# Kernel optimization log

Measured on AMD Instinct MI355X. Metric: run time of the kernel, lower is better.

The kernel has to match this reference:

```python
import jax, jax.numpy as jnp
import numpy as np

K = 16  # top-k affinities kept per current-frame pixel (init arg k)


def setup_inputs() -> dict:
    key = jax.random.key(0)
    k1, k2 = jax.random.split(key)
    B, C, H, W = 2, 256, 64, 64
    N = H * W
    cur_prev_aff = jax.random.normal(k1, (B, N, N), dtype=jnp.float32)
    feat = jax.random.normal(k2, (B, C, H, W), dtype=jnp.float32)
    return {"cur_prev_aff": cur_prev_aff, "feat": feat}


def reference(cur_prev_aff, feat):
    # cur_prev_aff: [B, N, N] affinity from each current pixel i to each prev pixel j
    # feat:         [B, C, H, W] previous-frame features, N = H*W
    B, C, H, W = feat.shape
    N = H * W
    # top-k affinity masking per current pixel
    vals, idx = jax.lax.top_k(cur_prev_aff, K)      # [B, N, K]
    w = jax.nn.softmax(vals, axis=-1)               # normalized masked affinities (masked_cpa)
    # gather prev-frame features at top-k locations and weighted-sum
    feat_t = feat.reshape(B, C, N).transpose(0, 2, 1)        # [B, N, C]
    gathered = jax.vmap(lambda f, ix: f[ix])(feat_t, idx)    # [B, N, K, C]
    out = jnp.einsum('bnk,bnkc->bnc', w, gathered)           # [B, N, C]
    return out.transpose(0, 2, 1).reshape(B, C, H, W)
```

## Files before the change

### kernel.cpp

```cpp
#include <hip/hip_runtime.h>

#define N_PIX 4096
#define N_CH 256
#define KSEL 16
#define SCAP 64

__device__ __forceinline__ unsigned f2key(float f) {
  unsigned u = __float_as_uint(f);
  return u ^ ((unsigned)((int)u >> 31) | 0x80000000u);
}
__device__ __forceinline__ float key2f(unsigned k) {
  unsigned u = (k & 0x80000000u) ? (k ^ 0x80000000u) : ~k;
  return __uint_as_float(u);
}
__device__ __forceinline__ unsigned umax2(unsigned a, unsigned b) { return a > b ? a : b; }

__global__ void transpose_feat_kernel(const float* __restrict__ feat,
                                      float* __restrict__ feat_t) {
  __shared__ float tile[32][33];
  const int b = blockIdx.z;
  const int n0 = blockIdx.x * 32;
  const int c0 = blockIdx.y * 32;
  const int tx = threadIdx.x, ty = threadIdx.y;
  const float* src = feat + (size_t)b * N_CH * N_PIX;
  float* dst = feat_t + (size_t)b * N_PIX * N_CH;
#pragma unroll
  for (int j = 0; j < 32; j += 8)
    tile[ty + j][tx] = src[(size_t)(c0 + ty + j) * N_PIX + n0 + tx];
  __syncthreads();
#pragma unroll
  for (int j = 0; j < 32; j += 8)
    dst[(size_t)(n0 + ty + j) * N_CH + c0 + tx] = tile[tx][ty + j];
}

template <bool FT>
__global__ __launch_bounds__(256, 2) void topk_reg_kernel(
    const float* __restrict__ aff, const float* __restrict__ feat,
    float* __restrict__ out) {
  __shared__ uint2 s_slab[4][SCAP];
  __shared__ uint2 s_wj[4][KSEL];
  __shared__ float s_out[4][N_CH];

  const int tid = threadIdx.x;
  const int lane = tid & 63;
  const int w = tid >> 6;
  const int bid = blockIdx.x;
  const int rg = (bid & 7) * 256 + (bid >> 3);
  const int b = rg >> 10;
  const int i0 = (rg & 1023) * 4;
  const int row = rg * 4 + w;
  const unsigned long long lt = (1ull << lane) - 1ull;

  const float4* arow = (const float4*)(aff + (size_t)row * N_PIX);
  uint4 kv[16];
  unsigned m = 0;
#pragma unroll
  for (int q = 0; q < 16; ++q) {
    const float4 v = arow[q * 64 + lane];
    const unsigned k0 = f2key(v.x), k1 = f2key(v.y), k2 = f2key(v.z), k3 = f2key(v.w);
    kv[q].x = k0; kv[q].y = k1; kv[q].z = k2; kv[q].w = k3;
    m = umax2(m, umax2(umax2(k0, k1), umax2(k2, k3)));
  }

  const unsigned t = m >> 16;
  unsigned p1 = 0, need1 = KSEL;
#pragma unroll
  for (int bit = 15; bit >= 0; --bit) {
    const unsigned want = (p1 << 1) | 1u;
    const unsigned cnt = (unsigned)__popcll(__ballot((t >> bit) == want));
    const bool take = cnt >= need1;
    p1 = want - (take ? 0u : 1u);
    need1 = take ? need1 : need1 - cnt;
  }
  const unsigned thrK = p1 << 16;

  s_slab[w][lane] = make_uint2(0u, 0xFFFFFFFFu);

  unsigned base = 0;
#pragma unroll
  for (int q = 0; q < 16; ++q) {
    const unsigned kk[4] = {kv[q].x, kv[q].y, kv[q].z, kv[q].w};
#pragma unroll
    for (int c = 0; c < 4; ++c) {
      const bool sel = kk[c] >= thrK;
      const unsigned long long mk = __ballot(sel);
      if (sel) {
        const unsigned pos = base + (unsigned)__popcll(mk & lt);
        if (pos < SCAP)
          s_slab[w][pos] = make_uint2(kk[c], (unsigned)(q * 256 + lane * 4 + c));
      }
      base += (unsigned)__popcll(mk);
    }
  }

  if (__builtin_expect(base > SCAP, 0)) {
    unsigned p2 = 0, need2 = KSEL;
    for (int bit = 31; bit >= 0; --bit) {
      const unsigned want = (p2 << 1) | 1u;
      unsigned cnt = 0;
#pragma unroll
      for (int q = 0; q < 16; ++q) {
        cnt += (unsigned)__popcll(__ballot((kv[q].x >> bit) == want));
        cnt += (unsigned)__popcll(__ballot((kv[q].y >> bit) == want));
        cnt += (unsigned)__popcll(__ballot((kv[q].z >> bit) == want));
        cnt += (unsigned)__popcll(__ballot((kv[q].w >> bit) == want));
      }
      const bool take = cnt >= need2;
      p2 = want - (take ? 0u : 1u);
      need2 = take ? need2 : need2 - cnt;
    }
    s_slab[w][lane] = make_uint2(0u, 0xFFFFFFFFu);
    base = 0;
#pragma unroll
    for (int q = 0; q < 16; ++q) {
      const unsigned kk[4] = {kv[q].x, kv[q].y, kv[q].z, kv[q].w};
#pragma unroll
      for (int c = 0; c < 4; ++c) {
        const bool sel = kk[c] >= p2;
        const unsigned long long mk = __ballot(sel);
        if (sel) {
          const unsigned pos = base + (unsigned)__popcll(mk & lt);
          if (pos < SCAP)
            s_slab[w][pos] = make_uint2(kk[c], (unsigned)(q * 256 + lane * 4 + c));
        }
        base += (unsigned)__popcll(mk);
      }
    }
  }

  {
    const uint2 cc = s_slab[w][lane];
    const unsigned cv = cc.x;
    const unsigned cj = cc.y;
    unsigned p2 = 0, need2 = KSEL;
    bool early = false;
    int bit = 31;
    for (; bit >= 0; --bit) {
      const unsigned want = (p2 << 1) | 1u;
      const unsigned cnt = (unsigned)__popcll(__ballot((cv >> bit) == want));
      if (cnt >= need2) {
        p2 = want;
        if (cnt == need2) { early = true; break; }
      } else {
        need2 -= cnt;
        p2 <<= 1;
      }
    }
    bool win;
    float vref;
    if (early) {
      const unsigned thr2 = p2 << bit;
      win = cv >= thr2;
      vref = key2f(thr2);
    } else {
      win = cv > p2;
      vref = key2f(p2);
      bool tq = (cv == p2) && (cj != 0xFFFFFFFFu);
      for (unsigned q = 0; q < need2; ++q) {
        unsigned mi = tq ? cj : 0xFFFFFFFFu;
#pragma unroll
        for (int off = 32; off; off >>= 1) {
          const unsigned o = (unsigned)__shfl_xor((int)mi, off, 64);
          mi = o < mi ? o : mi;
        }
        if (tq && cj == mi) { win = true; tq = false; }
      }
    }
    const unsigned long long wm = __ballot(win);
    if (win) {
      const unsigned rk = (unsigned)__popcll(wm & lt);
      s_wj[w][rk] = make_uint2(__float_as_uint(__expf(key2f(cv) - vref)), cj);
    }
  }

  float ssum = 0.f;
#pragma unroll
  for (int k = 0; k < KSEL; ++k) ssum += __uint_as_float(s_wj[w][k].x);
  const float inv = 1.0f / ssum;

  float ax = 0.f, ay = 0.f, az = 0.f, aw2 = 0.f;
  if (FT) {
    const float* fb = feat + (size_t)b * N_PIX * N_CH + lane * 4;
#pragma unroll
    for (int k = 0; k < KSEL; ++k) {
      const uint2 tt = s_wj[w][k];
      const float ew = __uint_as_float(tt.x);
      const float4 f = *(const float4*)(fb + (size_t)tt.y * N_CH);
      ax += ew * f.x; ay += ew * f.y; az += ew * f.z; aw2 += ew * f.w;
    }
  } else {
    const float* fb = feat + (size_t)b * N_CH * N_PIX;
    const int c0s = lane * 4;
#pragma unroll
    for (int k = 0; k < KSEL; ++k) {
      const uint2 tt = s_wj[w][k];
      const float ew = __uint_as_float(tt.x);
      ax += ew * fb[(size_t)(c0s + 0) * N_PIX + tt.y];
      ay += ew * fb[(size_t)(c0s + 1) * N_PIX + tt.y];
      az += ew * fb[(size_t)(c0s + 2) * N_PIX + tt.y];
      aw2 += ew * fb[(size_t)(c0s + 3) * N_PIX + tt.y];
    }
  }
  float4 accv;
  accv.x = ax * inv; accv.y = ay * inv; accv.z = az * inv; accv.w = aw2 * inv;
  *(float4*)&s_out[w][lane * 4] = accv;

  __syncthreads();

  {
    const int c = tid;
    float4 o;
    o.x = s_out[0][c]; o.y = s_out[1][c]; o.z = s_out[2][c]; o.w = s_out[3][c];
    *(float4*)(out + ((size_t)(b * N_CH + c)) * N_PIX + i0) = o;
  }
}

extern "C" void kernel_launch(void* const* d_in, const int* in_sizes, int n_in,
                              void* d_out, int out_size, void* d_ws, size_t ws_size,
                              hipStream_t stream) {
  const float* aff = (const float*)d_in[0];
  const float* feat = (const float*)d_in[1];
  float* out = (float*)d_out;
  const size_t feat_t_bytes = (size_t)2 * N_PIX * N_CH * sizeof(float);
  if (ws_size >= feat_t_bytes) {
    float* feat_t = (float*)d_ws;
    dim3 tb(32, 8, 1);
    dim3 tg(N_PIX / 32, N_CH / 32, 2);
    transpose_feat_kernel<<<tg, tb, 0, stream>>>(feat, feat_t);
    topk_reg_kernel<true><<<2048, 256, 0, stream>>>(aff, feat_t, out);
  } else {
    topk_reg_kernel<false><<<2048, 256, 0, stream>>>(aff, feat, out);
  }
}
```

Measured before the change: 51.81 us.

## Process four rows per wave with double-buffered row loads and private candidate lists

Each wave now handles four consecutive affinity rows and double-buffers them in registers, so the next row's loads overlap the current row's selection. Candidate compaction first gathers up to four hits per lane into private shared slots and places them with a ballot-based prefix sum, instead of one ballot per element. The block-level transpose through shared memory is dropped in favour of direct scattered scalar stores, and the grid shrinks to 512 blocks. Costs are much higher register pressure from two 16-float4 buffers, fewer blocks to hide latency, and uncoalesced output writes.

Measured after the change: 58.31 us. 1.13x slower.

```diff
diff --git a/kernel.cpp b/kernel.cpp
--- a/kernel.cpp
+++ b/kernel.cpp
@@ -3,6 +3,7 @@
 #define N_PIX 4096
 #define N_CH 256
 #define KSEL 16
+#define PCAP 4
 #define SCAP 64
 
 __device__ __forceinline__ unsigned f2key(float f) {
@@ -34,185 +35,232 @@
 }
 
 template <bool FT>
-__global__ __launch_bounds__(256, 2) void topk_reg_kernel(
+__global__ __launch_bounds__(256, 2) void topk_pipe_kernel(
     const float* __restrict__ aff, const float* __restrict__ feat,
     float* __restrict__ out) {
+  __shared__ uint2 s_priv[4][64][PCAP];
   __shared__ uint2 s_slab[4][SCAP];
   __shared__ uint2 s_wj[4][KSEL];
-  __shared__ float s_out[4][N_CH];
 
   const int tid = threadIdx.x;
   const int lane = tid & 63;
   const int w = tid >> 6;
   const int bid = blockIdx.x;
-  const int rg = (bid & 7) * 256 + (bid >> 3);
-  const int b = rg >> 10;
-  const int i0 = (rg & 1023) * 4;
-  const int row = rg * 4 + w;
+  const int swz = (bid & 7) * 64 + (bid >> 3);
+  const int row0 = swz * 16 + w * 4;
+  const int b = row0 >> 12;
   const unsigned long long lt = (1ull << lane) - 1ull;
 
-  const float4* arow = (const float4*)(aff + (size_t)row * N_PIX);
-  uint4 kv[16];
-  unsigned m = 0;
-#pragma unroll
-  for (int q = 0; q < 16; ++q) {
-    const float4 v = arow[q * 64 + lane];
-    const unsigned k0 = f2key(v.x), k1 = f2key(v.y), k2 = f2key(v.z), k3 = f2key(v.w);
-    kv[q].x = k0; kv[q].y = k1; kv[q].z = k2; kv[q].w = k3;
-    m = umax2(m, umax2(umax2(k0, k1), umax2(k2, k3)));
-  }
-
-  const unsigned t = m >> 16;
-  unsigned p1 = 0, need1 = KSEL;
-#pragma unroll
-  for (int bit = 15; bit >= 0; --bit) {
-    const unsigned want = (p1 << 1) | 1u;
-    const unsigned cnt = (unsigned)__popcll(__ballot((t >> bit) == want));
-    const bool take = cnt >= need1;
-    p1 = want - (take ? 0u : 1u);
-    need1 = take ? need1 : need1 - cnt;
-  }
-  const unsigned thrK = p1 << 16;
-
-  s_slab[w][lane] = make_uint2(0u, 0xFFFFFFFFu);
-
-  unsigned base = 0;
-#pragma unroll
-  for (int q = 0; q < 16; ++q) {
-    const unsigned kk[4] = {kv[q].x, kv[q].y, kv[q].z, kv[q].w};
-#pragma unroll
-    for (int c = 0; c < 4; ++c) {
-      const bool sel = kk[c] >= thrK;
-      const unsigned long long mk = __ballot(sel);
-      if (sel) {
-        const unsigned pos = base + (unsigned)__popcll(mk & lt);
-        if (pos < SCAP)
-          s_slab[w][pos] = make_uint2(kk[c], (unsigned)(q * 256 + lane * 4 + c));
-      }
-      base += (unsigned)__popcll(mk);
-    }
-  }
-
-  if (__builtin_expect(base > SCAP, 0)) {
-    unsigned p2 = 0, need2 = KSEL;
-    for (int bit = 31; bit >= 0; --bit) {
-      const unsigned want = (p2 << 1) | 1u;
-      unsigned cnt = 0;
-#pragma unroll
-      for (int q = 0; q < 16; ++q) {
-        cnt += (unsigned)__popcll(__ballot((kv[q].x >> bit) == want));
-        cnt += (unsigned)__popcll(__ballot((kv[q].y >> bit) == want));
-        cnt += (unsigned)__popcll(__ballot((kv[q].z >> bit) == want));
-        cnt += (unsigned)__popcll(__ballot((kv[q].w >> bit) == want));
-      }
-      const bool take = cnt >= need2;
-      p2 = want - (take ? 0u : 1u);
-      need2 = take ? need2 : need2 - cnt;
-    }
+  const float* fb = FT ? (feat + (size_t)b * N_PIX * N_CH + lane * 4)
+                       : (feat + (size_t)b * N_CH * N_PIX);
+
+  auto process = [&](const float4 (&fv)[16], int row) {
+    uint4 kv[16];
+    unsigned m = 0;
+#pragma unroll
+    for (int q = 0; q < 16; ++q) {
+      const unsigned k0 = f2key(fv[q].x), k1 = f2key(fv[q].y);
+      const unsigned k2 = f2key(fv[q].z), k3 = f2key(fv[q].w);
+      kv[q].x = k0; kv[q].y = k1; kv[q].z = k2; kv[q].w = k3;
+      m = umax2(m, umax2(umax2(k0, k1), umax2(k2, k3)));
+    }
+
+    const unsigned t = m >> 16;
+    unsigned p1 = 0, need1 = KSEL;
+#pragma unroll
+    for (int bit = 15; bit >= 0; --bit) {
+      const unsigned want = (p1 << 1) | 1u;
+      const unsigned cnt = (unsigned)__popcll(__ballot((t >> bit) == want));
+      const bool take = cnt >= need1;
+      p1 = want - (take ? 0u : 1u);
+      need1 = take ? need1 : need1 - cnt;
+    }
+    const unsigned thrK = p1 << 16;
+
     s_slab[w][lane] = make_uint2(0u, 0xFFFFFFFFu);
-    base = 0;
+
+    unsigned cl = 0;
 #pragma unroll
     for (int q = 0; q < 16; ++q) {
       const unsigned kk[4] = {kv[q].x, kv[q].y, kv[q].z, kv[q].w};
 #pragma unroll
       for (int c = 0; c < 4; ++c) {
-        const bool sel = kk[c] >= p2;
-        const unsigned long long mk = __ballot(sel);
-        if (sel) {
-          const unsigned pos = base + (unsigned)__popcll(mk & lt);
-          if (pos < SCAP)
-            s_slab[w][pos] = make_uint2(kk[c], (unsigned)(q * 256 + lane * 4 + c));
-        }
-        base += (unsigned)__popcll(mk);
-      }
-    }
-  }
-
-  {
-    const uint2 cc = s_slab[w][lane];
-    const unsigned cv = cc.x;
-    const unsigned cj = cc.y;
-    unsigned p2 = 0, need2 = KSEL;
-    bool early = false;
-    int bit = 31;
-    for (; bit >= 0; --bit) {
-      const unsigned want = (p2 << 1) | 1u;
-      const unsigned cnt = (unsigned)__popcll(__ballot((cv >> bit) == want));
-      if (cnt >= need2) {
-        p2 = want;
-        if (cnt == need2) { early = true; break; }
+        if (kk[c] >= thrK) {
+          if (cl < PCAP)
+            s_priv[w][lane][cl] =
+                make_uint2(kk[c], (unsigned)(q * 256 + lane * 4 + c));
+          ++cl;
+        }
+      }
+    }
+
+    unsigned total;
+    if (__builtin_expect(__ballot(cl > PCAP) == 0ull, 1)) {
+      const unsigned long long b0 = __ballot(cl & 1u);
+      const unsigned long long b1 = __ballot(cl & 2u);
+      const unsigned long long b2 = __ballot(cl & 4u);
+      const unsigned start = (unsigned)__popcll(b0 & lt) +
+                             2u * (unsigned)__popcll(b1 & lt) +
+                             4u * (unsigned)__popcll(b2 & lt);
+      total = (unsigned)__popcll(b0) + 2u * (unsigned)__popcll(b1) +
+              4u * (unsigned)__popcll(b2);
+      for (unsigned c = 0; c < cl; ++c) {
+        const uint2 tt = s_priv[w][lane][c];
+        if (start + c < SCAP) s_slab[w][start + c] = tt;
+      }
+    } else {
+      unsigned base = 0;
+#pragma unroll
+      for (int q = 0; q < 16; ++q) {
+        const unsigned kk[4] = {kv[q].x, kv[q].y, kv[q].z, kv[q].w};
+#pragma unroll
+        for (int c = 0; c < 4; ++c) {
+          const bool sel = kk[c] >= thrK;
+          const unsigned long long mk = __ballot(sel);
+          if (sel) {
+            const unsigned pos = base + (unsigned)__popcll(mk & lt);
+            if (pos < SCAP)
+              s_slab[w][pos] =
+                  make_uint2(kk[c], (unsigned)(q * 256 + lane * 4 + c));
+          }
+          base += (unsigned)__popcll(mk);
+        }
+      }
+      total = base;
+    }
+
+    if (__builtin_expect(total > SCAP, 0)) {
+      unsigned p2 = 0, need2 = KSEL;
+      for (int bit = 31; bit >= 0; --bit) {
+        const unsigned want = (p2 << 1) | 1u;
+        unsigned cnt = 0;
+#pragma unroll
+        for (int q = 0; q < 16; ++q) {
+          cnt += (unsigned)__popcll(__ballot((kv[q].x >> bit) == want));
+          cnt += (unsigned)__popcll(__ballot((kv[q].y >> bit) == want));
+          cnt += (unsigned)__popcll(__ballot((kv[q].z >> bit) == want));
+          cnt += (unsigned)__popcll(__ballot((kv[q].w >> bit) == want));
+        }
+        const bool take = cnt >= need2;
+        p2 = want - (take ? 0u : 1u);
+        need2 = take ? need2 : need2 - cnt;
+      }
+      s_slab[w][lane] = make_uint2(0u, 0xFFFFFFFFu);
+      unsigned base = 0;
+#pragma unroll
+      for (int q = 0; q < 16; ++q) {
+        const unsigned kk[4] = {kv[q].x, kv[q].y, kv[q].z, kv[q].w};
+#pragma unroll
+        for (int c = 0; c < 4; ++c) {
+          const bool sel = kk[c] >= p2;
+          const unsigned long long mk = __ballot(sel);
+          if (sel) {
+            const unsigned pos = base + (unsigned)__popcll(mk & lt);
+            if (pos < SCAP)
+              s_slab[w][pos] =
+                  make_uint2(kk[c], (unsigned)(q * 256 + lane * 4 + c));
+          }
+          base += (unsigned)__popcll(mk);
+        }
+      }
+    }
+
+    {
+      const uint2 cc = s_slab[w][lane];
+      const unsigned cv = cc.x;
+      const unsigned cj = cc.y;
+      unsigned p2 = 0, need2 = KSEL;
+      bool early = false;
+      int bit = 31;
+      for (; bit >= 0; --bit) {
+        const unsigned want = (p2 << 1) | 1u;
+        const unsigned cnt = (unsigned)__popcll(__ballot((cv >> bit) == want));
+        if (cnt >= need2) {
+          p2 = want;
+          if (cnt == need2) { early = true; break; }
+        } else {
+          need2 -= cnt;
+          p2 <<= 1;
+        }
+      }
+      bool win;
+      float vref;
+      if (early) {
+        const unsigned thr2 = p2 << bit;
+        win = cv >= thr2;
+        vref = key2f(thr2);
       } else {
-        need2 -= cnt;
-        p2 <<= 1;
-      }
-    }
-    bool win;
-    float vref;
-    if (early) {
-      const unsigned thr2 = p2 << bit;
-      win = cv >= thr2;
-      vref = key2f(thr2);
+        win = cv > p2;
+        vref = key2f(p2);
+        bool tq = (cv == p2) && (cj != 0xFFFFFFFFu);
+        for (unsigned q = 0; q < need2; ++q) {
+          unsigned mi = tq ? cj : 0xFFFFFFFFu;
+#pragma unroll
+          for (int off = 32; off; off >>= 1) {
+            const unsigned o = (unsigned)__shfl_xor((int)mi, off, 64);
+            mi = o < mi ? o : mi;
+          }
+          if (tq && cj == mi) { win = true; tq = false; }
+        }
+      }
+      const unsigned long long wm = __ballot(win);
+      if (win) {
+        const unsigned rk = (unsigned)__popcll(wm & lt);
+        s_wj[w][rk] = make_uint2(__float_as_uint(__expf(key2f(cv) - vref)), cj);
+      }
+    }
+
+    float ssum = 0.f;
+    float ax = 0.f, ay = 0.f, az = 0.f, aw2 = 0.f;
+    if (FT) {
+#pragma unroll
+      for (int k = 0; k < KSEL; ++k) {
+        const uint2 tt = s_wj[w][k];
+        const float ew = __uint_as_float(tt.x);
+        ssum += ew;
+        const float4 f = *(const float4*)(fb + (size_t)tt.y * N_CH);
+        ax += ew * f.x; ay += ew * f.y; az += ew * f.z; aw2 += ew * f.w;
+      }
     } else {
-      win = cv > p2;
-      vref = key2f(p2);
-      bool tq = (cv == p2) && (cj != 0xFFFFFFFFu);
-      for (unsigned q = 0; q < need2; ++q) {
-        unsigned mi = tq ? cj : 0xFFFFFFFFu;
-#pragma unroll
-        for (int off = 32; off; off >>= 1) {
-          const unsigned o = (unsigned)__shfl_xor((int)mi, off, 64);
-          mi = o < mi ? o : mi;
-        }
-        if (tq && cj == mi) { win = true; tq = false; }
-      }
-    }
-    const unsigned long long wm = __ballot(win);
-    if (win) {
-      const unsigned rk = (unsigned)__popcll(wm & lt);
-      s_wj[w][rk] = make_uint2(__float_as_uint(__expf(key2f(cv) - vref)), cj);
-    }
-  }
-
-  float ssum = 0.f;
-#pragma unroll
-  for (int k = 0; k < KSEL; ++k) ssum += __uint_as_float(s_wj[w][k].x);
-  const float inv = 1.0f / ssum;
-
-  float ax = 0.f, ay = 0.f, az = 0.f, aw2 = 0.f;
-  if (FT) {
-    const float* fb = feat + (size_t)b * N_PIX * N_CH + lane * 4;
-#pragma unroll
-    for (int k = 0; k < KSEL; ++k) {
-      const uint2 tt = s_wj[w][k];
-      const float ew = __uint_as_float(tt.x);
-      const float4 f = *(const float4*)(fb + (size_t)tt.y * N_CH);
-      ax += ew * f.x; ay += ew * f.y; az += ew * f.z; aw2 += ew * f.w;
-    }
-  } else {
-    const float* fb = feat + (size_t)b * N_CH * N_PIX;
-    const int c0s = lane * 4;
-#pragma unroll
-    for (int k = 0; k < KSEL; ++k) {
-      const uint2 tt = s_wj[w][k];
-      const float ew = __uint_as_float(tt.x);
-      ax += ew * fb[(size_t)(c0s + 0) * N_PIX + tt.y];
-      ay += ew * fb[(size_t)(c0s + 1) * N_PIX + tt.y];
-      az += ew * fb[(size_t)(c0s + 2) * N_PIX + tt.y];
-      aw2 += ew * fb[(size_t)(c0s + 3) * N_PIX + tt.y];
-    }
-  }
-  float4 accv;
-  accv.x = ax * inv; accv.y = ay * inv; accv.z = az * inv; accv.w = aw2 * inv;
-  *(float4*)&s_out[w][lane * 4] = accv;
-
-  __syncthreads();
-
-  {
-    const int c = tid;
-    float4 o;
-    o.x = s_out[0][c]; o.y = s_out[1][c]; o.z = s_out[2][c]; o.w = s_out[3][c];
-    *(float4*)(out + ((size_t)(b * N_CH + c)) * N_PIX + i0) = o;
-  }
+      const int c0s = lane * 4;
+#pragma unroll
+      for (int k = 0; k < KSEL; ++k) {
+        const uint2 tt = s_wj[w][k];
+        const float ew = __uint_as_float(tt.x);
+        ssum += ew;
+        ax += ew * fb[(size_t)(c0s + 0) * N_PIX + tt.y];
+        ay += ew * fb[(size_t)(c0s + 1) * N_PIX + tt.y];
+        az += ew * fb[(size_t)(c0s + 2) * N_PIX + tt.y];
+        aw2 += ew * fb[(size_t)(c0s + 3) * N_PIX + tt.y];
+      }
+    }
+    const float inv = 1.0f / ssum;
+    const int i = row & (N_PIX - 1);
+    float* op = out + ((size_t)(b * N_CH + lane * 4)) * N_PIX + i;
+    op[0] = ax * inv;
+    op[N_PIX] = ay * inv;
+    op[2 * N_PIX] = az * inv;
+    op[3 * N_PIX] = aw2 * inv;
+  };
+
+  const float4* a0 = (const float4*)(aff + (size_t)(row0 + 0) * N_PIX);
+  const float4* a1 = (const float4*)(aff + (size_t)(row0 + 1) * N_PIX);
+  const float4* a2 = (const float4*)(aff + (size_t)(row0 + 2) * N_PIX);
+  const float4* a3 = (const float4*)(aff + (size_t)(row0 + 3) * N_PIX);
+
+  float4 fvA[16], fvB[16];
+#pragma unroll
+  for (int q = 0; q < 16; ++q) fvA[q] = a0[q * 64 + lane];
+#pragma unroll
+  for (int q = 0; q < 16; ++q) fvB[q] = a1[q * 64 + lane];
+  process(fvA, row0 + 0);
+#pragma unroll
+  for (int q = 0; q < 16; ++q) fvA[q] = a2[q * 64 + lane];
+  process(fvB, row0 + 1);
+#pragma unroll
+  for (int q = 0; q < 16; ++q) fvB[q] = a3[q * 64 + lane];
+  process(fvA, row0 + 2);
+  process(fvB, row0 + 3);
 }
 
 extern "C" void kernel_launch(void* const* d_in, const int* in_sizes, int n_in,
@@ -227,8 +275,8 @@
     dim3 tb(32, 8, 1);
     dim3 tg(N_PIX / 32, N_CH / 32, 2);
     transpose_feat_kernel<<<tg, tb, 0, stream>>>(feat, feat_t);
-    topk_reg_kernel<true><<<2048, 256, 0, stream>>>(aff, feat_t, out);
+    topk_pipe_kernel<true><<<512, 256, 0, stream>>>(aff, feat_t, out);
   } else {
-    topk_reg_kernel<false><<<2048, 256, 0, stream>>>(aff, feat, out);
+    topk_pipe_kernel<false><<<512, 256, 0, stream>>>(aff, feat, out);
   }
 }
```

## Pack 16-bit key prefixes in registers and compact candidates per lane

Applied to the files above, without the earlier changes.

Keeps only the high 16 bits of each affinity key, packed two per register, which halves the register footprint and allows raising launch bounds to four blocks per SM. Candidate selection now counts up to four hits per lane locally and compacts them with three ballots instead of 64 ballots. Only indices go into shared memory, and the full values are re-read from global memory for the final exact selection. Loads are double-buffered, and the overflow fallback rescans the row from global memory. The cost is extra global reads and a more complex slow path.

New measurement: 51.99 us. Within noise of the previous version (+0.3%).

```diff
diff --git a/kernel.cpp b/kernel.cpp
--- a/kernel.cpp
+++ b/kernel.cpp
@@ -34,10 +34,10 @@
 }
 
 template <bool FT>
-__global__ __launch_bounds__(256, 2) void topk_reg_kernel(
+__global__ __launch_bounds__(256, 4) void topk_pk_kernel(
     const float* __restrict__ aff, const float* __restrict__ feat,
     float* __restrict__ out) {
-  __shared__ uint2 s_slab[4][SCAP];
+  __shared__ unsigned s_slab[4][SCAP];
   __shared__ uint2 s_wj[4][KSEL];
   __shared__ float s_out[4][N_CH];
 
@@ -51,15 +51,33 @@
   const int row = rg * 4 + w;
   const unsigned long long lt = (1ull << lane) - 1ull;
 
-  const float4* arow = (const float4*)(aff + (size_t)row * N_PIX);
-  uint4 kv[16];
+  const float* arow_f = aff + (size_t)row * N_PIX;
+  const float4* arow = (const float4*)arow_f;
+
+  unsigned ph[32];
   unsigned m = 0;
-#pragma unroll
-  for (int q = 0; q < 16; ++q) {
-    const float4 v = arow[q * 64 + lane];
-    const unsigned k0 = f2key(v.x), k1 = f2key(v.y), k2 = f2key(v.z), k3 = f2key(v.w);
-    kv[q].x = k0; kv[q].y = k1; kv[q].z = k2; kv[q].w = k3;
-    m = umax2(m, umax2(umax2(k0, k1), umax2(k2, k3)));
+  float4 fvA[4], fvB[4];
+#pragma unroll
+  for (int r = 0; r < 4; ++r) fvA[r] = arow[r * 64 + lane];
+#pragma unroll
+  for (int bq = 0; bq < 4; ++bq) {
+    if (bq < 3) {
+#pragma unroll
+      for (int r = 0; r < 4; ++r)
+        fvB[r] = arow[((bq + 1) * 4 + r) * 64 + lane];
+    }
+#pragma unroll
+    for (int r = 0; r < 4; ++r) {
+      const int q = bq * 4 + r;
+      const float4 v = fvA[r];
+      const unsigned k0 = f2key(v.x), k1 = f2key(v.y);
+      const unsigned k2 = f2key(v.z), k3 = f2key(v.w);
+      m = umax2(m, umax2(umax2(k0, k1), umax2(k2, k3)));
+      ph[2 * q + 0] = (k1 & 0xFFFF0000u) | (k0 >> 16);
+      ph[2 * q + 1] = (k3 & 0xFFFF0000u) | (k2 >> 16);
+    }
+#pragma unroll
+    for (int r = 0; r < 4; ++r) fvA[r] = fvB[r];
   }
 
   const unsigned t = m >> 16;
@@ -72,66 +90,79 @@
     p1 = want - (take ? 0u : 1u);
     need1 = take ? need1 : need1 - cnt;
   }
-  const unsigned thrK = p1 << 16;
-
-  s_slab[w][lane] = make_uint2(0u, 0xFFFFFFFFu);
-
-  unsigned base = 0;
-#pragma unroll
-  for (int q = 0; q < 16; ++q) {
-    const unsigned kk[4] = {kv[q].x, kv[q].y, kv[q].z, kv[q].w};
-#pragma unroll
-    for (int c = 0; c < 4; ++c) {
-      const bool sel = kk[c] >= thrK;
-      const unsigned long long mk = __ballot(sel);
-      if (sel) {
-        const unsigned pos = base + (unsigned)__popcll(mk & lt);
-        if (pos < SCAP)
-          s_slab[w][pos] = make_uint2(kk[c], (unsigned)(q * 256 + lane * 4 + c));
-      }
-      base += (unsigned)__popcll(mk);
-    }
-  }
-
-  if (__builtin_expect(base > SCAP, 0)) {
-    unsigned p2 = 0, need2 = KSEL;
-    for (int bit = 31; bit >= 0; --bit) {
-      const unsigned want = (p2 << 1) | 1u;
-      unsigned cnt = 0;
-#pragma unroll
-      for (int q = 0; q < 16; ++q) {
-        cnt += (unsigned)__popcll(__ballot((kv[q].x >> bit) == want));
-        cnt += (unsigned)__popcll(__ballot((kv[q].y >> bit) == want));
-        cnt += (unsigned)__popcll(__ballot((kv[q].z >> bit) == want));
-        cnt += (unsigned)__popcll(__ballot((kv[q].w >> bit) == want));
-      }
-      const bool take = cnt >= need2;
-      p2 = want - (take ? 0u : 1u);
-      need2 = take ? need2 : need2 - cnt;
-    }
-    s_slab[w][lane] = make_uint2(0u, 0xFFFFFFFFu);
-    base = 0;
-#pragma unroll
-    for (int q = 0; q < 16; ++q) {
-      const unsigned kk[4] = {kv[q].x, kv[q].y, kv[q].z, kv[q].w};
-#pragma unroll
-      for (int c = 0; c < 4; ++c) {
-        const bool sel = kk[c] >= p2;
+  const unsigned T1 = p1;
+
+  s_slab[w][lane] = 0xFFFFFFFFu;
+
+  unsigned cl = 0, j0 = 0, j1 = 0, j2 = 0, j3 = 0;
+#pragma unroll
+  for (int p = 0; p < 32; ++p) {
+    const unsigned lo = ph[p] & 0xFFFFu;
+    const unsigned hi = ph[p] >> 16;
+    const unsigned jlo = (unsigned)((p >> 1) * 256 + lane * 4 + (p & 1) * 2);
+    if (lo >= T1) {
+      j3 = (cl == 3) ? jlo : j3; j2 = (cl == 2) ? jlo : j2;
+      j1 = (cl == 1) ? jlo : j1; j0 = (cl == 0) ? jlo : j0;
+      ++cl;
+    }
+    if (hi >= T1) {
+      const unsigned jhi = jlo + 1;
+      j3 = (cl == 3) ? jhi : j3; j2 = (cl == 2) ? jhi : j2;
+      j1 = (cl == 1) ? jhi : j1; j0 = (cl == 0) ? jhi : j0;
+      ++cl;
+    }
+  }
+
+  unsigned total;
+  if (__builtin_expect(__ballot(cl > 4) == 0ull, 1)) {
+    const unsigned long long c0m = __ballot(cl & 1u);
+    const unsigned long long c1m = __ballot(cl & 2u);
+    const unsigned long long c2m = __ballot(cl & 4u);
+    const unsigned start = (unsigned)__popcll(c0m & lt) +
+                           2u * (unsigned)__popcll(c1m & lt) +
+                           4u * (unsigned)__popcll(c2m & lt);
+    total = (unsigned)__popcll(c0m) + 2u * (unsigned)__popcll(c1m) +
+            4u * (unsigned)__popcll(c2m);
+    if (cl > 0 && start + 0 < SCAP) s_slab[w][start + 0] = j0;
+    if (cl > 1 && start + 1 < SCAP) s_slab[w][start + 1] = j1;
+    if (cl > 2 && start + 2 < SCAP) s_slab[w][start + 2] = j2;
+    if (cl > 3 && start + 3 < SCAP) s_slab[w][start + 3] = j3;
+  } else {
+    unsigned base = 0;
+#pragma unroll
+    for (int p = 0; p < 32; ++p) {
+      const unsigned lo = ph[p] & 0xFFFFu;
+      const unsigned hi = ph[p] >> 16;
+      const unsigned jlo = (unsigned)((p >> 1) * 256 + lane * 4 + (p & 1) * 2);
+      {
+        const bool sel = lo >= T1;
         const unsigned long long mk = __ballot(sel);
         if (sel) {
           const unsigned pos = base + (unsigned)__popcll(mk & lt);
-          if (pos < SCAP)
-            s_slab[w][pos] = make_uint2(kk[c], (unsigned)(q * 256 + lane * 4 + c));
+          if (pos < SCAP) s_slab[w][pos] = jlo;
         }
         base += (unsigned)__popcll(mk);
       }
-    }
-  }
-
-  {
-    const uint2 cc = s_slab[w][lane];
-    const unsigned cv = cc.x;
-    const unsigned cj = cc.y;
+      {
+        const bool sel = hi >= T1;
+        const unsigned long long mk = __ballot(sel);
+        if (sel) {
+          const unsigned pos = base + (unsigned)__popcll(mk & lt);
+          if (pos < SCAP) s_slab[w][pos] = jlo + 1;
+        }
+        base += (unsigned)__popcll(mk);
+      }
+    }
+    total = base;
+  }
+
+  if (__builtin_expect(total <= SCAP, 1)) {
+    const unsigned jj = s_slab[w][lane];
+    const bool valid = jj != 0xFFFFFFFFu;
+    const float fval = arow_f[valid ? jj : 0u];
+    const unsigned cv = valid ? f2key(fval) : 0u;
+    const unsigned cj = valid ? jj : 0xFFFFFFFFu;
+
     unsigned p2 = 0, need2 = KSEL;
     bool early = false;
     int bit = 31;
@@ -155,7 +186,7 @@
     } else {
       win = cv > p2;
       vref = key2f(p2);
-      bool tq = (cv == p2) && (cj != 0xFFFFFFFFu);
+      bool tq = (cv == p2) && valid;
       for (unsigned q = 0; q < need2; ++q) {
         unsigned mi = tq ? cj : 0xFFFFFFFFu;
 #pragma unroll
@@ -170,6 +201,60 @@
     if (win) {
       const unsigned rk = (unsigned)__popcll(wm & lt);
       s_wj[w][rk] = make_uint2(__float_as_uint(__expf(key2f(cv) - vref)), cj);
+    }
+  } else {
+    unsigned p2 = 0, need2 = KSEL;
+    for (int bit = 31; bit >= 0; --bit) {
+      const unsigned want = (p2 << 1) | 1u;
+      unsigned cnt = 0;
+      for (int q = 0; q < 16; ++q) {
+        float4 v = arow[q * 64 + lane];
+        cnt += (unsigned)__popcll(__ballot((f2key(v.x) >> bit) == want));
+        cnt += (unsigned)__popcll(__ballot((f2key(v.y) >> bit) == want));
+        cnt += (unsigned)__popcll(__ballot((f2key(v.z) >> bit) == want));
+        cnt += (unsigned)__popcll(__ballot((f2key(v.w) >> bit) == want));
+      }
+      const bool take = cnt >= need2;
+      p2 = want - (take ? 0u : 1u);
+      need2 = take ? need2 : need2 - cnt;
+    }
+    const float vref = key2f(p2);
+    unsigned rk = 0;
+    for (int q = 0; q < 16; ++q) {
+      float4 v = arow[q * 64 + lane];
+      const float fvv[4] = {v.x, v.y, v.z, v.w};
+      for (int c = 0; c < 4; ++c) {
+        const unsigned kk = f2key(fvv[c]);
+        const bool sel = kk > p2;
+        const unsigned long long mk = __ballot(sel);
+        if (sel) {
+          const unsigned pos = rk + (unsigned)__popcll(mk & lt);
+          if (pos < KSEL)
+            s_wj[w][pos] = make_uint2(__float_as_uint(__expf(fvv[c] - vref)),
+                                      (unsigned)(q * 256 + lane * 4 + c));
+        }
+        rk += (unsigned)__popcll(mk);
+      }
+    }
+    unsigned jprev = 0xFFFFFFFFu;
+    for (unsigned tq = rk; tq < KSEL; ++tq) {
+      unsigned mi = 0xFFFFFFFFu;
+      for (int q = 0; q < 16; ++q) {
+        float4 v = arow[q * 64 + lane];
+        const float fvv[4] = {v.x, v.y, v.z, v.w};
+        for (int c = 0; c < 4; ++c) {
+          const unsigned j = (unsigned)(q * 256 + lane * 4 + c);
+          if (f2key(fvv[c]) == p2 && (jprev == 0xFFFFFFFFu || j > jprev) && j < mi)
+            mi = j;
+        }
+      }
+#pragma unroll
+      for (int off = 32; off; off >>= 1) {
+        const unsigned o = (unsigned)__shfl_xor((int)mi, off, 64);
+        mi = o < mi ? o : mi;
+      }
+      if (lane == 0) s_wj[w][tq] = make_uint2(__float_as_uint(1.0f), mi);
+      jprev = mi;
     }
   }
 
@@ -227,8 +312,8 @@
     dim3 tb(32, 8, 1);
     dim3 tg(N_PIX / 32, N_CH / 32, 2);
     transpose_feat_kernel<<<tg, tb, 0, stream>>>(feat, feat_t);
-    topk_reg_kernel<true><<<2048, 256, 0, stream>>>(aff, feat_t, out);
+    topk_pk_kernel<true><<<2048, 256, 0, stream>>>(aff, feat_t, out);
   } else {
-    topk_reg_kernel<false><<<2048, 256, 0, stream>>>(aff, feat, out);
-  }
-}
+    topk_pk_kernel<false><<<2048, 256, 0, stream>>>(aff, feat, out);
+  }
+}
```
